# Optimization experiments

Measured on AMD Instinct MI355X. Metric: run time of the kernel, lower is better.

Reference implementation:

```python
import jax, jax.numpy as jnp
import numpy as np
import math

B, S, HID, H = 1, 512, 256, 8
D = HID // H
SCALE = 1.0 / math.sqrt(D)
PI = math.pi


def setup_inputs() -> dict:
    key = jax.random.key(0)
    ks = jax.random.split(key, 6)
    x = jax.random.normal(ks[0], (B, S, HID), dtype=jnp.float32)
    w = lambda k: jax.random.normal(k, (HID, HID), dtype=jnp.float32) * 0.02
    return {
        'x': x,
        'wq': w(ks[1]), 'bq': jnp.zeros((HID,), jnp.float32),
        'wk': w(ks[2]), 'bk': jnp.zeros((HID,), jnp.float32),
        'wv': w(ks[3]), 'bv': jnp.zeros((HID,), jnp.float32),
        'wo': w(ks[4]), 'bo': jnp.zeros((HID,), jnp.float32),
    }


def _split_heads(t):
    # [B,S,HID] -> [B,H,S,D]
    return t.reshape(B, S, H, D).transpose(0, 2, 1, 3)


def reference(x, wq, bq, wk, bk, wv, bv, wo, bo):
    # Linear projections (torch nn.Linear: x @ W.T + b)
    q = _split_heads(x @ wq.T + bq)
    k = _split_heads(x @ wk.T + bk)
    v = _split_heads(x @ wv.T + bv)

    omega = jax.nn.sigmoid(q) * PI      # [B,H,S,D]
    amplitude = jax.nn.sigmoid(k)       # [B,H,S,D]
    phase = jnp.tanh(v) * PI            # [B,H,S,D]

    # relative position i-j, [S,S]
    pos = (jnp.arange(S)[:, None] - jnp.arange(S)[None, :]).astype(jnp.float32)
    # wave interference tensor [B,H,S,D,S] (query i, dim d, key j)
    interaction = amplitude[..., None] * jnp.cos(
        omega[..., None] * pos[None, None, :, None, :] + phase[..., None])
    patterns = jax.nn.softmax(interaction * SCALE, axis=-1)  # softmax over keys j
    # contract over key positions: per-dim attention
    context = jnp.einsum('bhidj,bhjd->bhid', patterns, v)    # [B,H,S,D]
    context = context.transpose(0, 2, 1, 3).reshape(B, S, HID)
    return context @ wo.T + bo
```

## Files before the change

kernel.cpp:

```cpp
#include <hip/hip_runtime.h>
#include <math.h>

#define SEQ 512
#define HID 256
#define NH 8
#define DH 32
#define PI_F 3.14159265358979323846f
#define SCALE_F 0.17677669529663687f
#define LOG2E_F 1.4426950408889634f

#define OFF_OMEGA 0
#define OFF_AMP   131072
#define OFF_PHASE 262144
#define OFF_V     393216

__global__ __launch_bounds__(256) void gemm_qkv_act(
    const float* __restrict__ x,
    const float* __restrict__ wq, const float* __restrict__ bq,
    const float* __restrict__ wk, const float* __restrict__ bk,
    const float* __restrict__ wv, const float* __restrict__ bv,
    const float* __restrict__ bo,
    float* __restrict__ ws, float* __restrict__ out)
{
    const int b = blockIdx.x;
    const int which = b >> 6;
    const int t = b & 63;
    const int r0 = (t >> 3) * 64;
    const int c0 = (t & 7) * 32;
    const float* W = (which == 0) ? wq : (which == 1) ? wk : wv;
    const float* B = (which == 0) ? bq : (which == 1) ? bk : bv;

    __shared__ float xs[64][68];
    __shared__ float wls[32][68];

    const int tid = threadIdx.x;
    const int rg = tid >> 4, cg = tid & 15;

    {
        int base = b * 256 + tid;
        for (int idx = base; idx < SEQ * HID; idx += 192 * 256)
            out[idx] = bo[idx & 255];
    }

    const int arr = tid >> 4, af = tid & 15;
    float4 pa[4], pw[2];
#pragma unroll
    for (int it = 0; it < 4; it++)
        pa[it] = *(const float4*)(x + (r0 + arr + it * 16) * HID + 4 * af);
#pragma unroll
    for (int it = 0; it < 2; it++)
        pw[it] = *(const float4*)(W + (c0 + arr + it * 16) * HID + 4 * af);

    float acc[4][2];
#pragma unroll
    for (int i = 0; i < 4; i++) { acc[i][0] = 0.f; acc[i][1] = 0.f; }

    for (int k0 = 0; k0 < HID; k0 += 64) {
#pragma unroll
        for (int it = 0; it < 4; it++)
            *(float4*)&xs[arr + it * 16][4 * af] = pa[it];
#pragma unroll
        for (int it = 0; it < 2; it++)
            *(float4*)&wls[arr + it * 16][4 * af] = pw[it];
        __syncthreads();

        if (k0 + 64 < HID) {
#pragma unroll
            for (int it = 0; it < 4; it++)
                pa[it] = *(const float4*)(x + (r0 + arr + it * 16) * HID + k0 + 64 + 4 * af);
#pragma unroll
            for (int it = 0; it < 2; it++)
                pw[it] = *(const float4*)(W + (c0 + arr + it * 16) * HID + k0 + 64 + 4 * af);
        }

#pragma unroll
        for (int g = 0; g < 16; g++) {
            float4 wv0 = *(const float4*)&wls[2 * cg + 0][4 * g];
            float4 wv1 = *(const float4*)&wls[2 * cg + 1][4 * g];
#pragma unroll
            for (int i = 0; i < 4; i++) {
                float4 xv = *(const float4*)&xs[4 * rg + i][4 * g];
                acc[i][0] = fmaf(xv.x, wv0.x, acc[i][0]);
                acc[i][0] = fmaf(xv.y, wv0.y, acc[i][0]);
                acc[i][0] = fmaf(xv.z, wv0.z, acc[i][0]);
                acc[i][0] = fmaf(xv.w, wv0.w, acc[i][0]);
                acc[i][1] = fmaf(xv.x, wv1.x, acc[i][1]);
                acc[i][1] = fmaf(xv.y, wv1.y, acc[i][1]);
                acc[i][1] = fmaf(xv.z, wv1.z, acc[i][1]);
                acc[i][1] = fmaf(xv.w, wv1.w, acc[i][1]);
            }
        }
        __syncthreads();
    }

    const float b0 = B[c0 + 2 * cg + 0];
    const float b1 = B[c0 + 2 * cg + 1];
#pragma unroll
    for (int i = 0; i < 4; i++) {
        int row = r0 + 4 * rg + i;
#pragma unroll
        for (int j = 0; j < 2; j++) {
            float val = acc[i][j] + (j ? b1 : b0);
            int o = row * HID + c0 + 2 * cg + j;
            if (which == 0) {
                ws[OFF_OMEGA + o] = PI_F / (1.f + expf(-val));
            } else if (which == 1) {
                ws[OFF_AMP + o] = 1.f / (1.f + expf(-val));
            } else {
                ws[OFF_V + o] = val;
                ws[OFF_PHASE + o] = PI_F * tanhf(val);
            }
        }
    }
}

__global__ __launch_bounds__(256) void wave_attn_out(
    const float* __restrict__ ws, const float* __restrict__ wo,
    float* __restrict__ out)
{
    const int b  = blockIdx.x;
    const int i8 = b >> 3;
    const int h  = b & 7;
    const int il = threadIdx.x >> 5;
    const int d  = threadIdx.x & 31;
    const int i  = i8 * 8 + il;
    const int col = h * DH + d;
    const int tid = threadIdx.x;

    __shared__ float wo_l[256][33];
    __shared__ float ctx_l[8][33];

#pragma unroll
    for (int it = 0; it < 8; it++) {
        int idx = tid + it * 256;
        int c = idx >> 3, f = idx & 7;
        float4 wv = *(const float4*)(wo + c * HID + h * DH + 4 * f);
        wo_l[c][4 * f + 0] = wv.x;
        wo_l[c][4 * f + 1] = wv.y;
        wo_l[c][4 * f + 2] = wv.z;
        wo_l[c][4 * f + 3] = wv.w;
    }

    const float w  = ws[OFF_OMEGA + i * HID + col];
    const float aL = ws[OFF_AMP + i * HID + col] * (SCALE_F * LOG2E_F);
    const float ph = ws[OFF_PHASE + i * HID + col];
    const float* vcol = ws + OFF_V + col;

    float sw_, cw;
    sincosf(w, &sw_, &cw);
    float c2 = cw * cw - sw_ * sw_, s2 = 2.f * sw_ * cw;
    float c4 = c2 * c2 - s2 * s2,   s4 = 2.f * s2 * c2;

    float th0 = fmaf(w, (float)i, ph);
    float s0, cc0;
    sincosf(th0, &s0, &cc0);

    float pc[4], psn[4];
    pc[0] = cc0; psn[0] = s0;
#pragma unroll
    for (int k = 1; k < 4; k++) {
        float nc = pc[k - 1] * cw + psn[k - 1] * sw_;
        float ns = psn[k - 1] * cw - pc[k - 1] * sw_;
        pc[k] = nc; psn[k] = ns;
    }
    float p[4], q[4], den[4], num[4];
#pragma unroll
    for (int k = 0; k < 4; k++) {
        p[k] = aL * pc[k]; q[k] = aL * psn[k];
        den[k] = 0.f; num[k] = 0.f;
    }

#pragma unroll 4
    for (int t = 0; t < SEQ / 4; t++) {
        float v0 = vcol[(4 * t + 0) * HID];
        float v1 = vcol[(4 * t + 1) * HID];
        float v2v = vcol[(4 * t + 2) * HID];
        float v3 = vcol[(4 * t + 3) * HID];
        float e0 = __builtin_amdgcn_exp2f(p[0]);
        float e1 = __builtin_amdgcn_exp2f(p[1]);
        float e2 = __builtin_amdgcn_exp2f(p[2]);
        float e3 = __builtin_amdgcn_exp2f(p[3]);
        den[0] += e0; den[1] += e1; den[2] += e2; den[3] += e3;
        num[0] = fmaf(e0, v0, num[0]);
        num[1] = fmaf(e1, v1, num[1]);
        num[2] = fmaf(e2, v2v, num[2]);
        num[3] = fmaf(e3, v3, num[3]);
#pragma unroll
        for (int k = 0; k < 4; k++) {
            float np = p[k] * c4 + q[k] * s4;
            float nq = q[k] * c4 - p[k] * s4;
            p[k] = np; q[k] = nq;
        }
    }
    float denom = (den[0] + den[1]) + (den[2] + den[3]);
    float numer = (num[0] + num[1]) + (num[2] + num[3]);

    __syncthreads();
    ctx_l[il][d] = numer / denom;
    __syncthreads();

    float ctx_r[32];
#pragma unroll
    for (int kk = 0; kk < 32; kk++) ctx_r[kk] = ctx_l[il][kk];
#pragma unroll
    for (int m = 0; m < 8; m++) {
        const int c = d + 32 * m;
        float s = 0.f;
#pragma unroll
        for (int kk = 0; kk < 32; kk++)
            s = fmaf(ctx_r[kk], wo_l[c][kk], s);
        atomicAdd(&out[i * HID + c], s);
    }
}

extern "C" void kernel_launch(void* const* d_in, const int* in_sizes, int n_in,
                              void* d_out, int out_size, void* d_ws, size_t ws_size,
                              hipStream_t stream) {
    const float* x  = (const float*)d_in[0];
    const float* wq = (const float*)d_in[1];
    const float* bq = (const float*)d_in[2];
    const float* wk = (const float*)d_in[3];
    const float* bk = (const float*)d_in[4];
    const float* wv = (const float*)d_in[5];
    const float* bv = (const float*)d_in[6];
    const float* wo = (const float*)d_in[7];
    const float* bo = (const float*)d_in[8];

    float* ws  = (float*)d_ws;
    float* out = (float*)d_out;

    hipLaunchKernelGGL(gemm_qkv_act, dim3(192), dim3(256), 0, stream,
                       x, wq, bq, wk, bk, wv, bv, bo, ws, out);
    hipLaunchKernelGGL(wave_attn_out, dim3(512), dim3(256), 0, stream,
                       ws, wo, out);
}
```

Baseline: 109.4 us.

## Split-K QKV GEMM with atomic accumulation and move activations into attention kernel

The QKV projection becomes a split-K GEMM over 384 blocks, each computing a 64x64 tile for one quarter of K with a swizzled, transposed weight tile in shared memory, and accumulating raw products into a zeroed workspace with atomicAdd. Bias addition, sigmoid and tanh are moved into the attention kernel. The V bias is added to the context after the softmax rather than to each V element. This aims to fill more of the GPU during the projection, at the cost of an extra memset, float atomics and non-deterministic summation order.

New measurement: 118.3 us. 1.08x slower.

```diff
diff --git a/kernel.cpp b/kernel.cpp
--- a/kernel.cpp
+++ b/kernel.cpp
@@ -9,114 +9,96 @@
 #define SCALE_F 0.17677669529663687f
 #define LOG2E_F 1.4426950408889634f
 
-#define OFF_OMEGA 0
-#define OFF_AMP   131072
-#define OFF_PHASE 262144
-#define OFF_V     393216
-
-__global__ __launch_bounds__(256) void gemm_qkv_act(
+#define OFF_Q 0
+#define OFF_K 131072
+#define OFF_V 262144
+
+__device__ __forceinline__ void gemm_chunk(
+    const float* __restrict__ A, const float* __restrict__ W,
+    int r0, int c0, int k0, int tid, float (&acc)[4][4],
+    float* __restrict__ xs, float* __restrict__ wts)
+{
+#pragma unroll
+    for (int it = 0; it < 4; it++) {
+        int idx = tid + it * 256;
+        int rr = idx >> 4, f4 = idx & 15;
+        float4 av = *(const float4*)(A + (r0 + rr) * HID + k0 + 4 * f4);
+        *(float4*)&xs[rr * 68 + 4 * f4] = av;
+        float4 wv = *(const float4*)(W + (c0 + rr) * HID + k0 + 4 * f4);
+        int cw = rr ^ ((f4 & 7) << 2);
+        wts[(4 * f4 + 0) * 64 + cw] = wv.x;
+        wts[(4 * f4 + 1) * 64 + cw] = wv.y;
+        wts[(4 * f4 + 2) * 64 + cw] = wv.z;
+        wts[(4 * f4 + 3) * 64 + cw] = wv.w;
+    }
+    __syncthreads();
+    const int rg = tid >> 4, cgi = tid & 15;
+#pragma unroll
+    for (int g = 0; g < 16; g++) {
+        float xfa[4][4], wfa[4][4];
+#pragma unroll
+        for (int i = 0; i < 4; i++) {
+            float4 xv = *(const float4*)&xs[(4 * rg + i) * 68 + 4 * g];
+            xfa[i][0] = xv.x; xfa[i][1] = xv.y; xfa[i][2] = xv.z; xfa[i][3] = xv.w;
+        }
+        const int sw = (g & 7) << 2;
+#pragma unroll
+        for (int m = 0; m < 4; m++) {
+            float4 wv = *(const float4*)&wts[(4 * g + m) * 64 + ((4 * cgi) ^ sw)];
+            wfa[m][0] = wv.x; wfa[m][1] = wv.y; wfa[m][2] = wv.z; wfa[m][3] = wv.w;
+        }
+#pragma unroll
+        for (int m = 0; m < 4; m++)
+#pragma unroll
+            for (int i = 0; i < 4; i++)
+#pragma unroll
+                for (int j = 0; j < 4; j++)
+                    acc[i][j] = fmaf(xfa[i][m], wfa[m][j], acc[i][j]);
+    }
+    __syncthreads();
+}
+
+__global__ __launch_bounds__(256) void gemm_qkv_splitk(
     const float* __restrict__ x,
-    const float* __restrict__ wq, const float* __restrict__ bq,
-    const float* __restrict__ wk, const float* __restrict__ bk,
-    const float* __restrict__ wv, const float* __restrict__ bv,
-    const float* __restrict__ bo,
+    const float* __restrict__ wq, const float* __restrict__ wk,
+    const float* __restrict__ wv, const float* __restrict__ bo,
     float* __restrict__ ws, float* __restrict__ out)
 {
     const int b = blockIdx.x;
-    const int which = b >> 6;
-    const int t = b & 63;
-    const int r0 = (t >> 3) * 64;
-    const int c0 = (t & 7) * 32;
+    const int which = b >> 7;
+    const int t = (b >> 2) & 31;
+    const int ks = b & 3;
+    const int r0 = (t >> 2) * 64, c0 = (t & 3) * 64, k0 = ks * 64;
     const float* W = (which == 0) ? wq : (which == 1) ? wk : wv;
-    const float* B = (which == 0) ? bq : (which == 1) ? bk : bv;
-
-    __shared__ float xs[64][68];
-    __shared__ float wls[32][68];
+
+    for (int idx = b * 256 + threadIdx.x; idx < SEQ * HID; idx += 384 * 256)
+        out[idx] = bo[idx & 255];
+
+    __shared__ float xs[64 * 68];
+    __shared__ float wts[64 * 64];
 
     const int tid = threadIdx.x;
-    const int rg = tid >> 4, cg = tid & 15;
-
-    {
-        int base = b * 256 + tid;
-        for (int idx = base; idx < SEQ * HID; idx += 192 * 256)
-            out[idx] = bo[idx & 255];
-    }
-
-    const int arr = tid >> 4, af = tid & 15;
-    float4 pa[4], pw[2];
-#pragma unroll
-    for (int it = 0; it < 4; it++)
-        pa[it] = *(const float4*)(x + (r0 + arr + it * 16) * HID + 4 * af);
-#pragma unroll
-    for (int it = 0; it < 2; it++)
-        pw[it] = *(const float4*)(W + (c0 + arr + it * 16) * HID + 4 * af);
-
-    float acc[4][2];
-#pragma unroll
-    for (int i = 0; i < 4; i++) { acc[i][0] = 0.f; acc[i][1] = 0.f; }
-
-    for (int k0 = 0; k0 < HID; k0 += 64) {
-#pragma unroll
-        for (int it = 0; it < 4; it++)
-            *(float4*)&xs[arr + it * 16][4 * af] = pa[it];
-#pragma unroll
-        for (int it = 0; it < 2; it++)
-            *(float4*)&wls[arr + it * 16][4 * af] = pw[it];
-        __syncthreads();
-
-        if (k0 + 64 < HID) {
-#pragma unroll
-            for (int it = 0; it < 4; it++)
-                pa[it] = *(const float4*)(x + (r0 + arr + it * 16) * HID + k0 + 64 + 4 * af);
-#pragma unroll
-            for (int it = 0; it < 2; it++)
-                pw[it] = *(const float4*)(W + (c0 + arr + it * 16) * HID + k0 + 64 + 4 * af);
-        }
-
-#pragma unroll
-        for (int g = 0; g < 16; g++) {
-            float4 wv0 = *(const float4*)&wls[2 * cg + 0][4 * g];
-            float4 wv1 = *(const float4*)&wls[2 * cg + 1][4 * g];
-#pragma unroll
-            for (int i = 0; i < 4; i++) {
-                float4 xv = *(const float4*)&xs[4 * rg + i][4 * g];
-                acc[i][0] = fmaf(xv.x, wv0.x, acc[i][0]);
-                acc[i][0] = fmaf(xv.y, wv0.y, acc[i][0]);
-                acc[i][0] = fmaf(xv.z, wv0.z, acc[i][0]);
-                acc[i][0] = fmaf(xv.w, wv0.w, acc[i][0]);
-                acc[i][1] = fmaf(xv.x, wv1.x, acc[i][1]);
-                acc[i][1] = fmaf(xv.y, wv1.y, acc[i][1]);
-                acc[i][1] = fmaf(xv.z, wv1.z, acc[i][1]);
-                acc[i][1] = fmaf(xv.w, wv1.w, acc[i][1]);
-            }
-        }
-        __syncthreads();
-    }
-
-    const float b0 = B[c0 + 2 * cg + 0];
-    const float b1 = B[c0 + 2 * cg + 1];
-#pragma unroll
-    for (int i = 0; i < 4; i++) {
-        int row = r0 + 4 * rg + i;
-#pragma unroll
-        for (int j = 0; j < 2; j++) {
-            float val = acc[i][j] + (j ? b1 : b0);
-            int o = row * HID + c0 + 2 * cg + j;
-            if (which == 0) {
-                ws[OFF_OMEGA + o] = PI_F / (1.f + expf(-val));
-            } else if (which == 1) {
-                ws[OFF_AMP + o] = 1.f / (1.f + expf(-val));
-            } else {
-                ws[OFF_V + o] = val;
-                ws[OFF_PHASE + o] = PI_F * tanhf(val);
-            }
-        }
-    }
+    float acc[4][4];
+#pragma unroll
+    for (int i = 0; i < 4; i++)
+#pragma unroll
+        for (int j = 0; j < 4; j++) acc[i][j] = 0.f;
+
+    gemm_chunk(x, W, r0, c0, k0, tid, acc, xs, wts);
+
+    float* R = ws + which * 131072;
+    const int rg = tid >> 4, cgi = tid & 15;
+#pragma unroll
+    for (int i = 0; i < 4; i++)
+#pragma unroll
+        for (int j = 0; j < 4; j++)
+            atomicAdd(&R[(r0 + 4 * rg + i) * HID + c0 + 4 * cgi + j], acc[i][j]);
 }
 
 __global__ __launch_bounds__(256) void wave_attn_out(
     const float* __restrict__ ws, const float* __restrict__ wo,
-    float* __restrict__ out)
+    const float* __restrict__ bq, const float* __restrict__ bk,
+    const float* __restrict__ bv, float* __restrict__ out)
 {
     const int b  = blockIdx.x;
     const int i8 = b >> 3;
@@ -141,9 +123,14 @@
         wo_l[c][4 * f + 3] = wv.w;
     }
 
-    const float w  = ws[OFF_OMEGA + i * HID + col];
-    const float aL = ws[OFF_AMP + i * HID + col] * (SCALE_F * LOG2E_F);
-    const float ph = ws[OFF_PHASE + i * HID + col];
+    const float qr = ws[OFF_Q + i * HID + col] + bq[col];
+    const float kr = ws[OFF_K + i * HID + col] + bk[col];
+    const float bvc = bv[col];
+    const float vr = ws[OFF_V + i * HID + col] + bvc;
+
+    const float w  = PI_F / (1.f + expf(-qr));
+    const float aL = (SCALE_F * LOG2E_F) / (1.f + expf(-kr));
+    const float ph = PI_F * tanhf(vr);
     const float* vcol = ws + OFF_V + col;
 
     float sw_, cw;
@@ -196,7 +183,7 @@
     float numer = (num[0] + num[1]) + (num[2] + num[3]);
 
     __syncthreads();
-    ctx_l[il][d] = numer / denom;
+    ctx_l[il][d] = numer / denom + bvc;
     __syncthreads();
 
     float ctx_r[32];
@@ -229,8 +216,9 @@
     float* ws  = (float*)d_ws;
     float* out = (float*)d_out;
 
-    hipLaunchKernelGGL(gemm_qkv_act, dim3(192), dim3(256), 0, stream,
-                       x, wq, bq, wk, bk, wv, bv, bo, ws, out);
+    hipMemsetAsync(ws, 0, 3 * SEQ * HID * sizeof(float), stream);
+    hipLaunchKernelGGL(gemm_qkv_splitk, dim3(384), dim3(256), 0, stream,
+                       x, wq, wk, wv, bo, ws, out);
     hipLaunchKernelGGL(wave_attn_out, dim3(512), dim3(256), 0, stream,
-                       ws, wo, out);
-}
+                       ws, wo, bq, bk, bv, out);
+}
```
